# Kernel optimization log

Hardware: AMD Instinct MI355X
Metric: run time of the kernel (lower is better)

The kernel has to match this reference:

```python
import jax, jax.numpy as jnp
import numpy as np

D_MODEL = 1024
D_STATE = 32
D_CONV = 4
D_INNER = 2 * D_MODEL          # mamba default expand=2
DT_RANK = D_MODEL // 16        # 'auto' -> ceil(d_model/16)
BATCH, SEQ = 4, 2048
LN_EPS = 1e-5


def setup_inputs() -> dict:
    key = jax.random.key(0)
    ks = jax.random.split(key, 8)
    s = 0.02
    # S4D-real init for A_log, as in mamba_ssm
    A_log = jnp.log(jnp.tile(jnp.arange(1, D_STATE + 1, dtype=jnp.float32)[None, :], (D_INNER, 1)))
    return {
        "x": jax.random.normal(ks[0], (BATCH, SEQ, D_MODEL), jnp.float32),
        "in_proj_w": jax.random.normal(ks[1], (D_MODEL, 2 * D_INNER), jnp.float32) * s,
        "conv_w": jax.random.normal(ks[2], (D_INNER, D_CONV), jnp.float32) * s,
        "conv_b": jnp.zeros((D_INNER,), jnp.float32),
        "x_proj_w": jax.random.normal(ks[3], (D_INNER, DT_RANK + 2 * D_STATE), jnp.float32) * s,
        "dt_proj_w": jax.random.normal(ks[4], (DT_RANK, D_INNER), jnp.float32) * s,
        "dt_proj_b": jax.random.uniform(ks[5], (D_INNER,), jnp.float32, -4.0, -2.0),  # softplus -> small dt
        "A_log": A_log,
        "D": jnp.ones((D_INNER,), jnp.float32),
        "out_proj_w": jax.random.normal(ks[6], (D_INNER, D_MODEL), jnp.float32) * s,
        "ln_gamma": jnp.ones((D_MODEL,), jnp.float32),
        "ln_beta": jnp.zeros((D_MODEL,), jnp.float32),
    }


def reference(x, in_proj_w, conv_w, conv_b, x_proj_w, dt_proj_w, dt_proj_b,
              A_log, D, out_proj_w, ln_gamma, ln_beta):
    Bb, Ll, _ = x.shape
    # in_proj -> split into ssm branch (xi) and gate (z)
    xz = x @ in_proj_w                              # [B,L,2*Di]
    xi, z = jnp.split(xz, 2, axis=-1)               # each [B,L,Di]

    # causal depthwise conv1d (kernel D_CONV), left-padded, truncated to L
    xp = jnp.pad(xi, ((0, 0), (D_CONV - 1, 0), (0, 0)))
    xc = conv_b
    for k in range(D_CONV):
        xc = xc + xp[:, k:k + Ll, :] * conv_w[None, None, :, k]
    xi = jax.nn.silu(xc)                            # [B,L,Di]

    # x_proj -> dt, B, C
    dbc = xi @ x_proj_w                             # [B,L,dt_rank+2*S]
    dt = dbc[..., :DT_RANK]
    Bm = dbc[..., DT_RANK:DT_RANK + D_STATE]        # [B,L,S]
    Cm = dbc[..., DT_RANK + D_STATE:]               # [B,L,S]
    delta = jax.nn.softplus(dt @ dt_proj_w + dt_proj_b)  # [B,L,Di]

    A = -jnp.exp(A_log)                             # [Di,S]

    def step(h, inp):
        dl, bt, ct, ut = inp                        # [B,Di],[B,S],[B,S],[B,Di]
        dA = jnp.exp(dl[..., None] * A)             # [B,Di,S]
        h = dA * h + (dl * ut)[..., None] * bt[:, None, :]
        y = jnp.einsum('bds,bs->bd', h, ct)
        return h, y

    h0 = jnp.zeros((Bb, D_INNER, D_STATE), x.dtype)
    xs = (delta.transpose(1, 0, 2), Bm.transpose(1, 0, 2),
          Cm.transpose(1, 0, 2), xi.transpose(1, 0, 2))
    _, ys = jax.lax.scan(step, h0, xs)              # ys: [L,B,Di]

    y = ys.transpose(1, 0, 2) + xi * D              # skip term u*D
    y = y * jax.nn.silu(z)                          # gate
    out = y @ out_proj_w                            # [B,L,d_model]

    # LayerNorm(d_model)
    mu = out.mean(-1, keepdims=True)
    var = out.var(-1, keepdims=True)
    return (out - mu) / jnp.sqrt(var + LN_EPS) * ln_gamma + ln_beta
```

## Files before the change

kernel.cpp:

```cpp
#include <hip/hip_runtime.h>
#include <math.h>

#define D_MODEL 1024
#define D_STATE 32
#define D_CONV  4
#define D_INNER 2048
#define DT_RANK 64
#define BATCH   4
#define SEQ     2048
#define NTOK    (BATCH*SEQ)
#define DBC_N   (DT_RANK + 2*D_STATE)
#define NC      64
#define CL      (SEQ/NC)
#define KSPLIT  8
#define LOG2E   1.4426950408889634f

typedef unsigned short u16;
typedef short bf16x8 __attribute__((ext_vector_type(8)));
typedef float f32x4  __attribute__((ext_vector_type(4)));

__device__ __forceinline__ float bf2f(u16 u){
  return __uint_as_float(((unsigned)u) << 16);
}
__device__ __forceinline__ u16 f2bf(float f){
  unsigned u = __float_as_uint(f);
  return (u16)((u + 0x7fffu + ((u >> 16) & 1u)) >> 16);
}
__device__ __forceinline__ float sigmoidf_(float x){ return 1.f/(1.f+__expf(-x)); }
__device__ __forceinline__ float exp2_fast(float x){
  float r;
  asm("v_exp_f32 %0, %1" : "=v"(r) : "v"(x));
  return r;
}

typedef __attribute__((address_space(3))) void       lds_v;
typedef const __attribute__((address_space(1))) void gl_v;
#define GLOAD_LDS16(g, l) \
  __builtin_amdgcn_global_load_lds((gl_v*)(g), (lds_v*)(l), 16, 0, 0)

template<int MODE>
__global__ __launch_bounds__(256)
void mfma_gemm(int K,
               const u16* __restrict__ A, int lda,
               const u16* __restrict__ B, int ldb,
               void* __restrict__ C1, int ldc,
               u16*  __restrict__ C2,
               const float* __restrict__ bias)
{
  __shared__ u16 As[128*32];
  __shared__ u16 Bs[128*32];
  const int tid  = threadIdx.x;
  const int lane = tid & 63;
  const int wave = tid >> 6;
  const int wm = (wave>>1)*64, wn = (wave&1)*64;
  const int m0 = blockIdx.y*128, n0 = blockIdx.x*128;
  const size_t koff = (MODE==3) ? (size_t)blockIdx.z*K : 0;

  const int srow = tid >> 2;
  const int scs  = (((tid & 3) ^ ((srow >> 1) & 3)) * 8);

  const u16* Ag = A + (size_t)(m0 + srow)*lda + scs + koff;
  const u16* Bg = B + (size_t)(n0 + srow)*ldb + scs + koff;

  const int fr = lane & 15;
  const int fq = lane >> 4;
  const int sx = (fr >> 1) & 3;
  const int rdoff = ((fq ^ sx) * 8);
  f32x4 acc[4][4] = {};

  u16* as0 = &As[tid*8];
  u16* as1 = &As[2048 + tid*8];
  u16* bs0 = &Bs[tid*8];
  u16* bs1 = &Bs[2048 + tid*8];

  for (int k0=0; k0<K; k0+=32){
    GLOAD_LDS16(Ag + k0,                    as0);
    GLOAD_LDS16(Ag + (size_t)64*lda + k0,   as1);
    GLOAD_LDS16(Bg + k0,                    bs0);
    GLOAD_LDS16(Bg + (size_t)64*ldb + k0,   bs1);
    __syncthreads();

    bf16x8 af[4], bfr[4];
    #pragma unroll
    for (int i=0;i<4;i++){
      af[i]  = *(const bf16x8*)&As[(wm + i*16 + fr)*32 + rdoff];
      bfr[i] = *(const bf16x8*)&Bs[(wn + i*16 + fr)*32 + rdoff];
    }
    #pragma unroll
    for (int mi=0;mi<4;mi++)
      #pragma unroll
      for (int ni=0;ni<4;ni++)
        acc[mi][ni] = __builtin_amdgcn_mfma_f32_16x16x32_bf16(
            af[mi], bfr[ni], acc[mi][ni], 0, 0, 0);
    __syncthreads();
  }

  float* Cf = (float*)C1;
  if (MODE==3) Cf += (size_t)blockIdx.z*((size_t)NTOK*DBC_N);

  const bool second = (MODE==2) && (n0 >= D_INNER);
  #pragma unroll
  for (int mi=0;mi<4;mi++){
    #pragma unroll
    for (int ni=0;ni<4;ni++){
      int col = n0 + wn + ni*16 + fr;
      #pragma unroll
      for (int r=0;r<4;r++){
        int row = m0 + wm + mi*16 + fq*4 + r;
        float v = acc[mi][ni][r];
        if (MODE==0 || MODE==3){
          Cf[(size_t)row*ldc + col] = v;
        } else if (MODE==4){
          v += bias[col];
          v = (v > 20.f) ? v : log1pf(__expf(v));
          Cf[(size_t)row*ldc + col] = v;
        } else {
          if (second) C2[(size_t)row*D_INNER + (col - D_INNER)] = f2bf(v);
          else        Cf[(size_t)row*D_INNER + col] = v;
        }
      }
    }
  }
}

__global__ __launch_bounds__(256)
void cvt_f32_bf16(const float* __restrict__ in, u16* __restrict__ out)
{
  size_t i = (size_t)blockIdx.x*256 + threadIdx.x;
  float4 v = ((const float4*)in)[i];
  ushort4 o;
  o.x=f2bf(v.x); o.y=f2bf(v.y); o.z=f2bf(v.z); o.w=f2bf(v.w);
  ((ushort4*)out)[i] = o;
}

__global__ __launch_bounds__(256)
void transpose_cvt(const float* __restrict__ in, u16* __restrict__ out,
                   int R, int C)
{
  __shared__ float tile[64][65];
  const int bc = blockIdx.x*64, br = blockIdx.y*64;
  const int tx = threadIdx.x & 63, ty = threadIdx.x >> 6;
  #pragma unroll
  for (int i=0;i<16;i++){
    int r = ty + i*4;
    tile[r][tx] = in[(size_t)(br+r)*C + bc+tx];
  }
  __syncthreads();
  #pragma unroll
  for (int i=0;i<16;i++){
    int r = ty + i*4;
    out[(size_t)(bc+r)*R + br+tx] = f2bf(tile[tx][r]);
  }
}

__global__ __launch_bounds__(256)
void reduce_pk(const float* __restrict__ part, float* __restrict__ dbc,
               u16* __restrict__ dtbf)
{
  size_t i = (size_t)blockIdx.x*256 + threadIdx.x;
  const size_t stride4 = (size_t)NTOK*DBC_N/4;
  float4 s = ((const float4*)part)[i];
  #pragma unroll
  for (int z=1; z<KSPLIT; ++z){
    float4 v = ((const float4*)part)[z*stride4 + i];
    s.x+=v.x; s.y+=v.y; s.z+=v.z; s.w+=v.w;
  }
  ((float4*)dbc)[i] = s;
  int j = (int)(i & 31);
  if (j < 16){
    size_t row = i >> 5;
    ushort4 o;
    o.x=f2bf(s.x); o.y=f2bf(s.y); o.z=f2bf(s.z); o.w=f2bf(s.w);
    *(ushort4*)(dtbf + row*DT_RANK + 4*j) = o;
  }
}

__global__ __launch_bounds__(256)
void conv_silu_kernel(const float* __restrict__ xi_raw,
                      const float* __restrict__ conv_w,
                      const float* __restrict__ conv_b,
                      float* __restrict__ xi_post,
                      u16*   __restrict__ xi_bf)
{
  size_t idx = (size_t)blockIdx.x*256 + threadIdx.x;
  int d = (int)(idx % D_INNER);
  size_t bt = idx / D_INNER;
  int t = (int)(bt % SEQ);
  size_t b = bt / SEQ;
  const float* xi = xi_raw + b*(size_t)SEQ*D_INNER;
  float accv = conv_b[d];
  #pragma unroll
  for (int k=0;k<D_CONV;k++){
    int tt = t + k - (D_CONV-1);
    if (tt >= 0) accv += xi[(size_t)tt*D_INNER + d] * conv_w[d*D_CONV + k];
  }
  float res = accv * sigmoidf_(accv);
  xi_post[idx] = res;
  xi_bf[idx]   = f2bf(res);
}

__global__ __launch_bounds__(256)
void scan_part1(const float* __restrict__ dbc,
                const float* __restrict__ delta,
                const float* __restrict__ u,
                const float* __restrict__ A_log,
                float* __restrict__ q,
                float* __restrict__ sumdl_buf)
{
  const int ndg  = D_INNER/256;
  const int dgrp = blockIdx.x % ndg;
  const int c    = (blockIdx.x / ndg) % NC;
  const int b    =  blockIdx.x / (ndg*NC);
  const int d    = dgrp*256 + threadIdx.x;

  const float* Ap = A_log + (size_t)d*D_STATE;
  const float base = -__expf(Ap[0]) * LOG2E;
  bool fastp = true;
  #pragma unroll
  for (int s=1; s<D_STATE; ++s){
    float a2 = -__expf(Ap[s]) * LOG2E;
    float ideal = base * (float)(s+1);
    fastp = fastp && (fabsf(a2 - ideal) <= 1e-4f*fabsf(ideal));
  }

  const size_t tok0 = (size_t)b*SEQ + (size_t)c*CL;
  const float* dptr = delta + tok0*D_INNER + d;
  const float* uptr = u     + tok0*D_INNER + d;
  const float* dbcp = dbc   + tok0*DBC_N;

  float h[D_STATE] = {};
  float sumdl = 0.f;

  if (fastp){
    for (int t=0; t<CL; ++t){
      float dl = dptr[(size_t)t*D_INNER];
      float uu = uptr[(size_t)t*D_INNER];
      sumdl += dl;
      float w  = dl*uu;
      float E  = exp2_fast(dl*base);
      float E2 = E*E, E3 = E2*E, E4 = E2*E2;
      float P  = 1.f;
      const float4* B4 = (const float4*)(dbcp + (size_t)t*DBC_N + DT_RANK);
      #pragma unroll
      for (int g=0; g<8; ++g){
        float4 Bv = B4[g];
        float m0 = P*E, m1 = P*E2, m2 = P*E3, m3 = P*E4;
        h[4*g+0] = m0*h[4*g+0] + w*Bv.x;
        h[4*g+1] = m1*h[4*g+1] + w*Bv.y;
        h[4*g+2] = m2*h[4*g+2] + w*Bv.z;
        h[4*g+3] = m3*h[4*g+3] + w*Bv.w;
        P = m3;
      }
    }
  } else {
    float A2[D_STATE];
    #pragma unroll
    for (int g=0; g<8; ++g){
      float4 al = *(const float4*)(Ap + 4*g);
      A2[4*g+0] = -__expf(al.x)*LOG2E; A2[4*g+1] = -__expf(al.y)*LOG2E;
      A2[4*g+2] = -__expf(al.z)*LOG2E; A2[4*g+3] = -__expf(al.w)*LOG2E;
    }
    for (int t=0; t<CL; ++t){
      float dl = dptr[(size_t)t*D_INNER];
      float uu = uptr[(size_t)t*D_INNER];
      sumdl += dl;
      float w = dl*uu;
      const float4* B4 = (const float4*)(dbcp + (size_t)t*DBC_N + DT_RANK);
      #pragma unroll
      for (int g=0; g<8; ++g){
        float4 Bv = B4[g];
        h[4*g+0] = exp2_fast(dl*A2[4*g+0])*h[4*g+0] + w*Bv.x;
        h[4*g+1] = exp2_fast(dl*A2[4*g+1])*h[4*g+1] + w*Bv.y;
        h[4*g+2] = exp2_fast(dl*A2[4*g+2])*h[4*g+2] + w*Bv.z;
        h[4*g+3] = exp2_fast(dl*A2[4*g+3])*h[4*g+3] + w*Bv.w;
      }
    }
  }

  float* qp = q + (((size_t)b*NC + c)*D_INNER + d)*D_STATE;
  #pragma unroll
  for (int g=0; g<8; ++g)
    ((float4*)qp)[g] = make_float4(h[4*g+0],h[4*g+1],h[4*g+2],h[4*g+3]);
  sumdl_buf[((size_t)b*NC + c)*D_INNER + d] = sumdl;
}

__global__ __launch_bounds__(256)
void scan_combine(float* __restrict__ q,
                  const float* __restrict__ sumdl_buf,
                  const float* __restrict__ A_log)
{
  size_t idx = (size_t)blockIdx.x*256 + threadIdx.x;
  int s = (int)(idx % D_STATE);
  size_t dd = idx / D_STATE;
  int d = (int)(dd % D_INNER);
  int b = (int)(dd / D_INNER);

  const float As2 = -__expf(A_log[(size_t)d*D_STATE + s]) * LOG2E;
  float H = 0.f;
  for (int c=0; c<NC; ++c){
    size_t off = (((size_t)b*NC + c)*D_INNER + d)*D_STATE + s;
    float tmp = q[off];
    q[off] = H;
    H = exp2_fast(As2 * sumdl_buf[((size_t)b*NC + c)*D_INNER + d]) * H + tmp;
  }
}

__global__ __launch_bounds__(256)
void scan_part2(const float* __restrict__ dbc,
                const float* __restrict__ delta,
                const float* __restrict__ u,
                u16*         __restrict__ zy,
                const float* __restrict__ q,
                const float* __restrict__ A_log,
                const float* __restrict__ Dp)
{
  const int ndg  = D_INNER/256;
  const int dgrp = blockIdx.x % ndg;
  const int c    = (blockIdx.x / ndg) % NC;
  const int b    =  blockIdx.x / (ndg*NC);
  const int d    = dgrp*256 + threadIdx.x;

  const float* Ap = A_log + (size_t)d*D_STATE;
  const float base = -__expf(Ap[0]) * LOG2E;
  bool fastp = true;
  #pragma unroll
  for (int s=1; s<D_STATE; ++s){
    float a2 = -__expf(Ap[s]) * LOG2E;
    float ideal = base * (float)(s+1);
    fastp = fastp && (fabsf(a2 - ideal) <= 1e-4f*fabsf(ideal));
  }

  float h[D_STATE];
  const float* qp = q + (((size_t)b*NC + c)*D_INNER + d)*D_STATE;
  #pragma unroll
  for (int g=0; g<8; ++g){
    float4 hv = ((const float4*)qp)[g];
    h[4*g+0]=hv.x; h[4*g+1]=hv.y; h[4*g+2]=hv.z; h[4*g+3]=hv.w;
  }
  const float Dd = Dp[d];

  const size_t tok0 = (size_t)b*SEQ + (size_t)c*CL;
  const float* dptr = delta + tok0*D_INNER + d;
  const float* uptr = u     + tok0*D_INNER + d;
  u16*         zp   = zy    + tok0*D_INNER + d;
  const float* dbcp = dbc   + tok0*DBC_N;

  if (fastp){
    for (int t=0; t<CL; ++t){
      float dl = dptr[(size_t)t*D_INNER];
      float uu = uptr[(size_t)t*D_INNER];
      float zz = bf2f(zp[(size_t)t*D_INNER]);
      float w  = dl*uu;
      float E  = exp2_fast(dl*base);
      float E2 = E*E, E3 = E2*E, E4 = E2*E2;
      float P  = 1.f;
      const float4* B4 = (const float4*)(dbcp + (size_t)t*DBC_N + DT_RANK);
      const float4* C4 = B4 + 8;
      float y = 0.f;
      #pragma unroll
      for (int g=0; g<8; ++g){
        float4 Bv = B4[g];
        float4 Cv = C4[g];
        float m0 = P*E, m1 = P*E2, m2 = P*E3, m3 = P*E4;
        h[4*g+0] = m0*h[4*g+0] + w*Bv.x;  y += h[4*g+0]*Cv.x;
        h[4*g+1] = m1*h[4*g+1] + w*Bv.y;  y += h[4*g+1]*Cv.y;
        h[4*g+2] = m2*h[4*g+2] + w*Bv.z;  y += h[4*g+2]*Cv.z;
        h[4*g+3] = m3*h[4*g+3] + w*Bv.w;  y += h[4*g+3]*Cv.w;
        P = m3;
      }
      zp[(size_t)t*D_INNER] = f2bf((y + uu*Dd) * (zz * sigmoidf_(zz)));
    }
  } else {
    float A2[D_STATE];
    #pragma unroll
    for (int g=0; g<8; ++g){
      float4 al = *(const float4*)(Ap + 4*g);
      A2[4*g+0] = -__expf(al.x)*LOG2E; A2[4*g+1] = -__expf(al.y)*LOG2E;
      A2[4*g+2] = -__expf(al.z)*LOG2E; A2[4*g+3] = -__expf(al.w)*LOG2E;
    }
    for (int t=0; t<CL; ++t){
      float dl = dptr[(size_t)t*D_INNER];
      float uu = uptr[(size_t)t*D_INNER];
      float zz = bf2f(zp[(size_t)t*D_INNER]);
      float w  = dl*uu;
      const float4* B4 = (const float4*)(dbcp + (size_t)t*DBC_N + DT_RANK);
      const float4* C4 = B4 + 8;
      float y = 0.f;
      #pragma unroll
      for (int g=0; g<8; ++g){
        float4 Bv = B4[g];
        float4 Cv = C4[g];
        h[4*g+0] = exp2_fast(dl*A2[4*g+0])*h[4*g+0] + w*Bv.x;  y += h[4*g+0]*Cv.x;
        h[4*g+1] = exp2_fast(dl*A2[4*g+1])*h[4*g+1] + w*Bv.y;  y += h[4*g+1]*Cv.y;
        h[4*g+2] = exp2_fast(dl*A2[4*g+2])*h[4*g+2] + w*Bv.z;  y += h[4*g+2]*Cv.z;
        h[4*g+3] = exp2_fast(dl*A2[4*g+3])*h[4*g+3] + w*Bv.w;  y += h[4*g+3]*Cv.w;
      }
      zp[(size_t)t*D_INNER] = f2bf((y + uu*Dd) * (zz * sigmoidf_(zz)));
    }
  }
}

__global__ __launch_bounds__(256)
void ln_kernel(const float* __restrict__ in,
               float* __restrict__ out,
               const float* __restrict__ gamma,
               const float* __restrict__ beta)
{
  const int row = blockIdx.x;
  const float* p = in + (size_t)row*D_MODEL;
  float* q = out + (size_t)row*D_MODEL;
  float v[4]; float s=0.f, ss=0.f;
  #pragma unroll
  for (int i=0;i<4;i++){
    float x = p[i*256 + threadIdx.x];
    v[i]=x; s+=x; ss+=x*x;
  }
  #pragma unroll
  for (int off=32; off; off>>=1){
    s  += __shfl_xor(s,  off, 64);
    ss += __shfl_xor(ss, off, 64);
  }
  __shared__ float sw[4], ssw[4];
  const int wid = threadIdx.x >> 6;
  if ((threadIdx.x & 63) == 0){ sw[wid]=s; ssw[wid]=ss; }
  __syncthreads();
  s  = sw[0]+sw[1]+sw[2]+sw[3];
  ss = ssw[0]+ssw[1]+ssw[2]+ssw[3];
  const float mu  = s * (1.f/D_MODEL);
  const float var = ss * (1.f/D_MODEL) - mu*mu;
  const float inv = rsqrtf(var + 1e-5f);
  #pragma unroll
  for (int i=0;i<4;i++){
    int col = i*256 + threadIdx.x;
    q[col] = (v[i]-mu)*inv*gamma[col] + beta[col];
  }
}

extern "C" void kernel_launch(void* const* d_in, const int* in_sizes, int n_in,
                              void* d_out, int out_size, void* d_ws, size_t ws_size,
                              hipStream_t stream)
{
  const float* x          = (const float*)d_in[0];
  const float* in_proj_w  = (const float*)d_in[1];
  const float* conv_w     = (const float*)d_in[2];
  const float* conv_b     = (const float*)d_in[3];
  const float* x_proj_w   = (const float*)d_in[4];
  const float* dt_proj_w  = (const float*)d_in[5];
  const float* dt_proj_b  = (const float*)d_in[6];
  const float* A_log      = (const float*)d_in[7];
  const float* Dp         = (const float*)d_in[8];
  const float* out_proj_w = (const float*)d_in[9];
  const float* ln_gamma   = (const float*)d_in[10];
  const float* ln_beta    = (const float*)d_in[11];
  float* out = (float*)d_out;

  char* ws = (char*)d_ws;
  float* xi_raw  = (float*)(ws + 0);
  float* pkpart  = (float*)(ws + 0);
  float* deltab  = (float*)(ws + 0);
  float* preln   = (float*)(ws + 0);
  float* xi_post = (float*)(ws + (size_t) 67108864);
  u16*   zybuf   = (u16*)  (ws + (size_t)134217728);
  u16*   x_bf    = (u16*)  (ws + (size_t)167772160);
  float* dbc     = (float*)(ws + (size_t)167772160);
  u16*   xi_bf   = (u16*)  (ws + (size_t)171966464);
  float* qbuf    = (float*)(ws + (size_t)171966464);
  float* sumdl   = (float*)(ws + (size_t)239075328);
  u16*   w_inT   = (u16*)  (ws + (size_t)241172480);
  u16*   w_outT  = (u16*)  (ws + (size_t)249561088);
  u16*   x_projT = (u16*)  (ws + (size_t)253755392);
  u16*   dt_projT= (u16*)  (ws + (size_t)254279680);
  u16*   dtbf    = (u16*)  (ws + (size_t)254803968);

  cvt_f32_bf16<<<(NTOK*(size_t)D_MODEL)/1024, 256, 0, stream>>>(x, x_bf);
  { dim3 g(4096/64, 1024/64); transpose_cvt<<<g,256,0,stream>>>(in_proj_w,  w_inT,  1024, 4096); }
  { dim3 g(1024/64, 2048/64); transpose_cvt<<<g,256,0,stream>>>(out_proj_w, w_outT, 2048, 1024); }
  { dim3 g( 128/64, 2048/64); transpose_cvt<<<g,256,0,stream>>>(x_proj_w,   x_projT, 2048, 128); }
  { dim3 g(2048/64,   64/64); transpose_cvt<<<g,256,0,stream>>>(dt_proj_w,  dt_projT,  64, 2048); }

  {
    dim3 grid(2*D_INNER/128, NTOK/128);
    mfma_gemm<2><<<grid,256,0,stream>>>(D_MODEL,
        x_bf, D_MODEL, w_inT, D_MODEL, xi_raw, 0, zybuf, nullptr);
  }
  conv_silu_kernel<<<(NTOK*(size_t)D_INNER)/256,256,0,stream>>>(
      xi_raw, conv_w, conv_b, xi_post, xi_bf);

  {
    dim3 grid(DBC_N/128, NTOK/128, KSPLIT);
    mfma_gemm<3><<<grid,256,0,stream>>>(D_INNER/KSPLIT,
        xi_bf, D_INNER, x_projT, D_INNER, pkpart, DBC_N, nullptr, nullptr);
    reduce_pk<<<(NTOK*(size_t)DBC_N)/1024,256,0,stream>>>(pkpart, dbc, dtbf);
  }
  {
    dim3 grid(D_INNER/128, NTOK/128);
    mfma_gemm<4><<<grid,256,0,stream>>>(DT_RANK,
        dtbf, DT_RANK, dt_projT, DT_RANK, deltab, D_INNER, nullptr, dt_proj_b);
  }
  {
    dim3 grid1((D_INNER/256)*NC*BATCH);
    scan_part1<<<grid1,256,0,stream>>>(dbc, deltab, xi_post, A_log, qbuf, sumdl);
    scan_combine<<<(BATCH*(size_t)D_INNER*D_STATE)/256,256,0,stream>>>(qbuf, sumdl, A_log);
    scan_part2<<<grid1,256,0,stream>>>(dbc, deltab, xi_post, zybuf, qbuf, A_log, Dp);
  }
  {
    dim3 grid(D_MODEL/128, NTOK/128);
    mfma_gemm<0><<<grid,256,0,stream>>>(D_INNER,
        zybuf, D_INNER, w_outT, D_INNER, preln, D_MODEL, nullptr, nullptr);
  }
  ln_kernel<<<NTOK,256,0,stream>>>(preln, out, ln_gamma, ln_beta);
}
```

Baseline: 623.0 us.

## Store xi, u and delta intermediates in bf16 and halve scan chunk count

The in_proj GEMM now writes the xi half as bf16, and the conv/SiLU kernel reads bf16 and emits a single bf16 u buffer instead of fp32 plus bf16 copies. The delta GEMM also stores softplus output as bf16, so both scan passes read half-width delta and u streams. This cuts the memory traffic of these bandwidth-bound elementwise and scan stages, and the workspace layout is reorganised to match. NC drops from 64 to 32, giving longer sequential chunks and fewer scan blocks; both the reduced precision of delta and u and the lower parallelism carry risk.

Result: faster. 588.7 us (-5.5%).

```diff
diff --git a/kernel.cpp b/kernel.cpp
--- a/kernel.cpp
+++ b/kernel.cpp
@@ -10,7 +10,7 @@
 #define SEQ     2048
 #define NTOK    (BATCH*SEQ)
 #define DBC_N   (DT_RANK + 2*D_STATE)
-#define NC      64
+#define NC      32
 #define CL      (SEQ/NC)
 #define KSPLIT  8
 #define LOG2E   1.4426950408889634f
@@ -113,10 +113,10 @@
         } else if (MODE==4){
           v += bias[col];
           v = (v > 20.f) ? v : log1pf(__expf(v));
-          Cf[(size_t)row*ldc + col] = v;
+          ((u16*)C1)[(size_t)row*ldc + col] = f2bf(v);
         } else {
           if (second) C2[(size_t)row*D_INNER + (col - D_INNER)] = f2bf(v);
-          else        Cf[(size_t)row*D_INNER + col] = v;
+          else        ((u16*)C1)[(size_t)row*D_INNER + col]     = f2bf(v);
         }
       }
     }
@@ -176,33 +176,31 @@
 }
 
 __global__ __launch_bounds__(256)
-void conv_silu_kernel(const float* __restrict__ xi_raw,
+void conv_silu_kernel(const u16* __restrict__ xi_bf,
                       const float* __restrict__ conv_w,
                       const float* __restrict__ conv_b,
-                      float* __restrict__ xi_post,
-                      u16*   __restrict__ xi_bf)
+                      u16* __restrict__ u_bf)
 {
   size_t idx = (size_t)blockIdx.x*256 + threadIdx.x;
   int d = (int)(idx % D_INNER);
   size_t bt = idx / D_INNER;
   int t = (int)(bt % SEQ);
   size_t b = bt / SEQ;
-  const float* xi = xi_raw + b*(size_t)SEQ*D_INNER;
+  const u16* xi = xi_bf + b*(size_t)SEQ*D_INNER;
   float accv = conv_b[d];
   #pragma unroll
   for (int k=0;k<D_CONV;k++){
     int tt = t + k - (D_CONV-1);
-    if (tt >= 0) accv += xi[(size_t)tt*D_INNER + d] * conv_w[d*D_CONV + k];
+    if (tt >= 0) accv += bf2f(xi[(size_t)tt*D_INNER + d]) * conv_w[d*D_CONV + k];
   }
   float res = accv * sigmoidf_(accv);
-  xi_post[idx] = res;
-  xi_bf[idx]   = f2bf(res);
+  u_bf[idx] = f2bf(res);
 }
 
 __global__ __launch_bounds__(256)
 void scan_part1(const float* __restrict__ dbc,
-                const float* __restrict__ delta,
-                const float* __restrict__ u,
+                const u16*   __restrict__ delta,
+                const u16*   __restrict__ u,
                 const float* __restrict__ A_log,
                 float* __restrict__ q,
                 float* __restrict__ sumdl_buf)
@@ -224,8 +222,8 @@
   }
 
   const size_t tok0 = (size_t)b*SEQ + (size_t)c*CL;
-  const float* dptr = delta + tok0*D_INNER + d;
-  const float* uptr = u     + tok0*D_INNER + d;
+  const u16*   dptr = delta + tok0*D_INNER + d;
+  const u16*   uptr = u     + tok0*D_INNER + d;
   const float* dbcp = dbc   + tok0*DBC_N;
 
   float h[D_STATE] = {};
@@ -233,8 +231,8 @@
 
   if (fastp){
     for (int t=0; t<CL; ++t){
-      float dl = dptr[(size_t)t*D_INNER];
-      float uu = uptr[(size_t)t*D_INNER];
+      float dl = bf2f(dptr[(size_t)t*D_INNER]);
+      float uu = bf2f(uptr[(size_t)t*D_INNER]);
       sumdl += dl;
       float w  = dl*uu;
       float E  = exp2_fast(dl*base);
@@ -261,8 +259,8 @@
       A2[4*g+2] = -__expf(al.z)*LOG2E; A2[4*g+3] = -__expf(al.w)*LOG2E;
     }
     for (int t=0; t<CL; ++t){
-      float dl = dptr[(size_t)t*D_INNER];
-      float uu = uptr[(size_t)t*D_INNER];
+      float dl = bf2f(dptr[(size_t)t*D_INNER]);
+      float uu = bf2f(uptr[(size_t)t*D_INNER]);
       sumdl += dl;
       float w = dl*uu;
       const float4* B4 = (const float4*)(dbcp + (size_t)t*DBC_N + DT_RANK);
@@ -307,8 +305,8 @@
 
 __global__ __launch_bounds__(256)
 void scan_part2(const float* __restrict__ dbc,
-                const float* __restrict__ delta,
-                const float* __restrict__ u,
+                const u16*   __restrict__ delta,
+                const u16*   __restrict__ u,
                 u16*         __restrict__ zy,
                 const float* __restrict__ q,
                 const float* __restrict__ A_log,
@@ -340,15 +338,15 @@
   const float Dd = Dp[d];
 
   const size_t tok0 = (size_t)b*SEQ + (size_t)c*CL;
-  const float* dptr = delta + tok0*D_INNER + d;
-  const float* uptr = u     + tok0*D_INNER + d;
+  const u16*   dptr = delta + tok0*D_INNER + d;
+  const u16*   uptr = u     + tok0*D_INNER + d;
   u16*         zp   = zy    + tok0*D_INNER + d;
   const float* dbcp = dbc   + tok0*DBC_N;
 
   if (fastp){
     for (int t=0; t<CL; ++t){
-      float dl = dptr[(size_t)t*D_INNER];
-      float uu = uptr[(size_t)t*D_INNER];
+      float dl = bf2f(dptr[(size_t)t*D_INNER]);
+      float uu = bf2f(uptr[(size_t)t*D_INNER]);
       float zz = bf2f(zp[(size_t)t*D_INNER]);
       float w  = dl*uu;
       float E  = exp2_fast(dl*base);
@@ -379,8 +377,8 @@
       A2[4*g+2] = -__expf(al.z)*LOG2E; A2[4*g+3] = -__expf(al.w)*LOG2E;
     }
     for (int t=0; t<CL; ++t){
-      float dl = dptr[(size_t)t*D_INNER];
-      float uu = uptr[(size_t)t*D_INNER];
+      float dl = bf2f(dptr[(size_t)t*D_INNER]);
+      float uu = bf2f(uptr[(size_t)t*D_INNER]);
       float zz = bf2f(zp[(size_t)t*D_INNER]);
       float w  = dl*uu;
       const float4* B4 = (const float4*)(dbcp + (size_t)t*DBC_N + DT_RANK);
@@ -455,22 +453,21 @@
   float* out = (float*)d_out;
 
   char* ws = (char*)d_ws;
-  float* xi_raw  = (float*)(ws + 0);
+  u16*   x_bf    = (u16*)  (ws + 0);
   float* pkpart  = (float*)(ws + 0);
-  float* deltab  = (float*)(ws + 0);
-  float* preln   = (float*)(ws + 0);
-  float* xi_post = (float*)(ws + (size_t) 67108864);
-  u16*   zybuf   = (u16*)  (ws + (size_t)134217728);
-  u16*   x_bf    = (u16*)  (ws + (size_t)167772160);
+  u16*   xi_bf   = (u16*)  (ws + (size_t) 33554432);
+  float* qbuf    = (float*)(ws + (size_t) 33554432);
+  u16*   u_bf    = (u16*)  (ws + (size_t) 67108864);
+  u16*   zybuf   = (u16*)  (ws + (size_t)100663296);
+  u16*   delta_bf= (u16*)  (ws + (size_t)134217728);
   float* dbc     = (float*)(ws + (size_t)167772160);
-  u16*   xi_bf   = (u16*)  (ws + (size_t)171966464);
-  float* qbuf    = (float*)(ws + (size_t)171966464);
-  float* sumdl   = (float*)(ws + (size_t)239075328);
-  u16*   w_inT   = (u16*)  (ws + (size_t)241172480);
-  u16*   w_outT  = (u16*)  (ws + (size_t)249561088);
-  u16*   x_projT = (u16*)  (ws + (size_t)253755392);
-  u16*   dt_projT= (u16*)  (ws + (size_t)254279680);
-  u16*   dtbf    = (u16*)  (ws + (size_t)254803968);
+  u16*   dtbf    = (u16*)  (ws + (size_t)171966464);
+  float* sumdl   = (float*)(ws + (size_t)173015040);
+  float* preln   = (float*)(ws + (size_t)174063616);
+  u16*   w_inT   = (u16*)  (ws + (size_t)207618048);
+  u16*   w_outT  = (u16*)  (ws + (size_t)216006656);
+  u16*   x_projT = (u16*)  (ws + (size_t)220200960);
+  u16*   dt_projT= (u16*)  (ws + (size_t)220725248);
 
   cvt_f32_bf16<<<(NTOK*(size_t)D_MODEL)/1024, 256, 0, stream>>>(x, x_bf);
   { dim3 g(4096/64, 1024/64); transpose_cvt<<<g,256,0,stream>>>(in_proj_w,  w_inT,  1024, 4096); }
@@ -481,27 +478,27 @@
   {
     dim3 grid(2*D_INNER/128, NTOK/128);
     mfma_gemm<2><<<grid,256,0,stream>>>(D_MODEL,
-        x_bf, D_MODEL, w_inT, D_MODEL, xi_raw, 0, zybuf, nullptr);
+        x_bf, D_MODEL, w_inT, D_MODEL, xi_bf, 0, zybuf, nullptr);
   }
   conv_silu_kernel<<<(NTOK*(size_t)D_INNER)/256,256,0,stream>>>(
-      xi_raw, conv_w, conv_b, xi_post, xi_bf);
+      xi_bf, conv_w, conv_b, u_bf);
 
   {
     dim3 grid(DBC_N/128, NTOK/128, KSPLIT);
     mfma_gemm<3><<<grid,256,0,stream>>>(D_INNER/KSPLIT,
-        xi_bf, D_INNER, x_projT, D_INNER, pkpart, DBC_N, nullptr, nullptr);
+        u_bf, D_INNER, x_projT, D_INNER, pkpart, DBC_N, nullptr, nullptr);
     reduce_pk<<<(NTOK*(size_t)DBC_N)/1024,256,0,stream>>>(pkpart, dbc, dtbf);
   }
   {
     dim3 grid(D_INNER/128, NTOK/128);
     mfma_gemm<4><<<grid,256,0,stream>>>(DT_RANK,
-        dtbf, DT_RANK, dt_projT, DT_RANK, deltab, D_INNER, nullptr, dt_proj_b);
+        dtbf, DT_RANK, dt_projT, DT_RANK, delta_bf, D_INNER, nullptr, dt_proj_b);
   }
   {
     dim3 grid1((D_INNER/256)*NC*BATCH);
-    scan_part1<<<grid1,256,0,stream>>>(dbc, deltab, xi_post, A_log, qbuf, sumdl);
+    scan_part1<<<grid1,256,0,stream>>>(dbc, delta_bf, u_bf, A_log, qbuf, sumdl);
     scan_combine<<<(BATCH*(size_t)D_INNER*D_STATE)/256,256,0,stream>>>(qbuf, sumdl, A_log);
-    scan_part2<<<grid1,256,0,stream>>>(dbc, deltab, xi_post, zybuf, qbuf, A_log, Dp);
+    scan_part2<<<grid1,256,0,stream>>>(dbc, delta_bf, u_bf, zybuf, qbuf, A_log, Dp);
   }
   {
     dim3 grid(D_MODEL/128, NTOK/128);
```
